# Optimization experiments

Hardware: AMD Instinct MI355X
Metric: run time of the kernel (lower is better)

Reference implementation:

```python
import jax, jax.numpy as jnp
import numpy as np

N = 100_000      # n_nodes
E = 1_000_000    # n_edges (avg degree 10)
DIN = 64
DOUT = 64


def setup_inputs() -> dict:
    key = jax.random.key(0)
    k1, k2, k3, k4 = jax.random.split(key, 4)
    x = jax.random.normal(k1, (N, DIN), dtype=jnp.float32)
    edge_index = jax.random.randint(k2, (2, E), 0, N, dtype=jnp.int32)
    # GCNConv linear weight (glorot-ish scale) and bias
    W = jax.random.normal(k3, (DIN, DOUT), dtype=jnp.float32) * (1.0 / np.sqrt(DIN))
    b = jax.random.normal(k4, (DOUT,), dtype=jnp.float32) * 0.01
    return {"x": x, "edge_index": edge_index, "W": W, "b": b}


def reference(x, edge_index, W, b):
    n = x.shape[0]
    # linear transform first (PyG GCNConv: x = self.lin(x))
    h = x @ W  # [N, DOUT]
    # add self-loops
    loop = jnp.arange(n, dtype=edge_index.dtype)
    row = jnp.concatenate([edge_index[0], loop])  # source j
    col = jnp.concatenate([edge_index[1], loop])  # target i
    # symmetric normalization: deg computed on target index (PyG gcn_norm)
    deg = jax.ops.segment_sum(jnp.ones(row.shape[0], dtype=h.dtype), col, num_segments=n)
    dinv = jnp.where(deg > 0, jax.lax.rsqrt(deg), 0.0)
    norm = dinv[row] * dinv[col]  # [E+N]
    # gather source features, scale, scatter-add to targets
    out = jax.ops.segment_sum(norm[:, None] * h[row], col, num_segments=n)
    out = out + b
    # dropout is identity in eval mode; act = relu
    return jax.nn.relu(out)
```

## Files before the change

kernel.cpp:

```cpp
#include <hip/hip_runtime.h>
#include <hip/hip_bf16.h>

#define F 64
#define BK 128
#define CAP 4096
#define ECAP 2048
#define PA_BLOCKS 256

typedef __attribute__((ext_vector_type(8))) short bf16x8;
typedef __attribute__((ext_vector_type(4))) float f32x4;

static __device__ inline short f2bf_bits(float f) {
    union { __hip_bfloat16 b; short s; } cv;
    cv.b = __float2bfloat16(f);
    return cv.s;
}

__global__ void __launch_bounds__(256)
k1_kernel(const float* __restrict__ x, const float* __restrict__ W,
          __hip_bfloat16* __restrict__ h,
          const int* __restrict__ row, const int* __restrict__ col,
          int* __restrict__ bcursor, unsigned* __restrict__ bin,
          int n, int e, int ngemm, int K, int chunk) {
    __shared__ int smem[2048];
    int tid = threadIdx.x;

    if ((int)blockIdx.x < ngemm) {
        short* Wb = (short*)smem;
        for (int i = tid; i < F * F; i += 256) Wb[i] = f2bf_bits(W[i]);
        __syncthreads();
        int lane = tid & 63;
        int wv = tid >> 6;
        int quad = lane >> 4;
        int l16 = lane & 15;

        bf16x8 bfr[2][4];
#pragma unroll
        for (int ks = 0; ks < 2; ++ks)
#pragma unroll
            for (int nb = 0; nb < 4; ++nb) {
                bf16x8 f;
#pragma unroll
                for (int j = 0; j < 8; ++j)
                    f[j] = Wb[(ks * 32 + quad * 8 + j) * F + nb * 16 + l16];
                bfr[ks][nb] = f;
            }

        int blockbase = blockIdx.x * 256;
#pragma unroll
        for (int mt = 0; mt < 4; ++mt) {
            int trow = blockbase + (wv * 4 + mt) * 16;
            int ar = trow + l16;
            bf16x8 af0, af1;
            if (ar < n) {
                const float* xr = x + (size_t)ar * F + quad * 8;
                float4 v0 = ((const float4*)xr)[0];
                float4 v1 = ((const float4*)xr)[1];
                float4 v2 = ((const float4*)(xr + 32))[0];
                float4 v3 = ((const float4*)(xr + 32))[1];
                af0[0] = f2bf_bits(v0.x); af0[1] = f2bf_bits(v0.y);
                af0[2] = f2bf_bits(v0.z); af0[3] = f2bf_bits(v0.w);
                af0[4] = f2bf_bits(v1.x); af0[5] = f2bf_bits(v1.y);
                af0[6] = f2bf_bits(v1.z); af0[7] = f2bf_bits(v1.w);
                af1[0] = f2bf_bits(v2.x); af1[1] = f2bf_bits(v2.y);
                af1[2] = f2bf_bits(v2.z); af1[3] = f2bf_bits(v2.w);
                af1[4] = f2bf_bits(v3.x); af1[5] = f2bf_bits(v3.y);
                af1[6] = f2bf_bits(v3.z); af1[7] = f2bf_bits(v3.w);
            } else {
                af0 = (bf16x8)0; af1 = (bf16x8)0;
            }
            f32x4 acc[4];
#pragma unroll
            for (int nb = 0; nb < 4; ++nb) {
                acc[nb] = (f32x4)0.f;
                acc[nb] = __builtin_amdgcn_mfma_f32_16x16x32_bf16(af0, bfr[0][nb], acc[nb], 0, 0, 0);
                acc[nb] = __builtin_amdgcn_mfma_f32_16x16x32_bf16(af1, bfr[1][nb], acc[nb], 0, 0, 0);
            }
#pragma unroll
            for (int nb = 0; nb < 4; ++nb)
#pragma unroll
                for (int r = 0; r < 4; ++r) {
                    int grow = trow + quad * 4 + r;
                    if (grow < n)
                        h[(size_t)grow * F + nb * 16 + l16] = __float2bfloat16(acc[nb][r]);
                }
        }
    } else {
        int* lh = smem;
        int* lbase = smem + 1024;
        int pb = blockIdx.x - ngemm;
        int s = pb * chunk;
        int lim = min(s + chunk, e);
        for (int i = tid; i < K; i += 256) lh[i] = 0;
        __syncthreads();
        for (int i = s + tid; i < lim; i += 256) atomicAdd(&lh[col[i] >> 7], 1);
        __syncthreads();
        for (int i = tid; i < K; i += 256) {
            int c = lh[i];
            lbase[i] = c ? atomicAdd(&bcursor[i], c) : 0;
            lh[i] = 0;
        }
        __syncthreads();
        for (int i = s + tid; i < lim; i += 256) {
            int d = col[i];
            int bkt = d >> 7;
            int off = lbase[bkt] + atomicAdd(&lh[bkt], 1);
            if (off < CAP)
                bin[(size_t)bkt * CAP + off] = ((unsigned)row[i] << 7) | ((unsigned)d & 127u);
        }
    }
}

__global__ void __launch_bounds__(256)
dinv_kernel(const unsigned* __restrict__ bin, const int* __restrict__ bcursor,
            float* __restrict__ dinv, int n) {
    __shared__ int lcnt[BK];
    int tid = threadIdx.x;
    int b = blockIdx.x;
    int s = b * CAP;
    int cnt = min(bcursor[b], ECAP);
    if (tid < BK) lcnt[tid] = 0;
    __syncthreads();
    for (int p = tid; p < cnt; p += 256) atomicAdd(&lcnt[bin[s + p] & 127u], 1);
    __syncthreads();
    if (tid < BK) {
        int node = (b << 7) + tid;
        if (node < n) dinv[node] = rsqrtf((float)(lcnt[tid] + 1));
    }
}

__global__ void __launch_bounds__(256)
gather_kernel(const unsigned* __restrict__ bin, const int* __restrict__ bcursor,
              const float* __restrict__ dinv, const __hip_bfloat16* __restrict__ h,
              const float* __restrict__ bias, float* __restrict__ out, int n) {
    __shared__ unsigned ebuf[ECAP];
    __shared__ int ssrc[ECAP];
    __shared__ int lcnt[BK];
    __shared__ int sstart[BK];
    __shared__ int lcur[BK];
    __shared__ int sc[BK];
    __shared__ float sdinv[BK];
    int tid = threadIdx.x;
    int b = blockIdx.x;
    int base = b << 7;
    int s = b * CAP;
    int cnt = min(bcursor[b], ECAP);

    if (tid < BK) lcnt[tid] = 0;
    __syncthreads();
    for (int p = tid; p < cnt; p += 256) {
        unsigned u = bin[s + p];
        ebuf[p] = u;
        atomicAdd(&lcnt[u & 127u], 1);
    }
    __syncthreads();
    if (tid < BK) sc[tid] = lcnt[tid];
    __syncthreads();
    for (int off = 1; off < BK; off <<= 1) {
        int t = (tid < BK && tid >= off) ? sc[tid - off] : 0;
        __syncthreads();
        if (tid < BK) sc[tid] += t;
        __syncthreads();
    }
    if (tid < BK) {
        int c = lcnt[tid];
        int st = sc[tid] - c;
        sstart[tid] = st;
        lcur[tid] = st;
        sdinv[tid] = rsqrtf((float)(c + 1));
    }
    __syncthreads();
    for (int p = tid; p < cnt; p += 256) {
        unsigned u = ebuf[p];
        int pos = atomicAdd(&lcur[u & 127u], 1);
        ssrc[pos] = (int)(u >> 7);
    }
    __syncthreads();

    int g = tid >> 3, cl = tid & 7;
    const uint4* h8 = (const uint4*)h;
#pragma unroll
    for (int r = 0; r < 4; ++r) {
        int ln = r * 32 + g;
        int node = base + ln;
        if (node >= n) continue;
        float di = sdinv[ln];
        float a0 = 0.f, a1 = 0.f, a2 = 0.f, a3 = 0.f,
              a4 = 0.f, a5 = 0.f, a6 = 0.f, a7 = 0.f;
        {
            uint4 hv = h8[(size_t)node * 8 + cl];
            a0 = di * __uint_as_float(hv.x << 16);
            a1 = di * __uint_as_float(hv.x & 0xffff0000u);
            a2 = di * __uint_as_float(hv.y << 16);
            a3 = di * __uint_as_float(hv.y & 0xffff0000u);
            a4 = di * __uint_as_float(hv.z << 16);
            a5 = di * __uint_as_float(hv.z & 0xffff0000u);
            a6 = di * __uint_as_float(hv.w << 16);
            a7 = di * __uint_as_float(hv.w & 0xffff0000u);
        }
        int p = sstart[ln];
        int pend = p + lcnt[ln];
        for (; p < pend; ++p) {
            int src = ssrc[p];
            float w = dinv[src];
            uint4 hv = h8[(size_t)src * 8 + cl];
            a0 += w * __uint_as_float(hv.x << 16);
            a1 += w * __uint_as_float(hv.x & 0xffff0000u);
            a2 += w * __uint_as_float(hv.y << 16);
            a3 += w * __uint_as_float(hv.y & 0xffff0000u);
            a4 += w * __uint_as_float(hv.z << 16);
            a5 += w * __uint_as_float(hv.z & 0xffff0000u);
            a6 += w * __uint_as_float(hv.w << 16);
            a7 += w * __uint_as_float(hv.w & 0xffff0000u);
        }
        float4 b0 = ((const float4*)bias)[cl * 2];
        float4 b1 = ((const float4*)bias)[cl * 2 + 1];
        float4 r0, r1;
        r0.x = di * a0 + b0.x; r0.y = di * a1 + b0.y;
        r0.z = di * a2 + b0.z; r0.w = di * a3 + b0.w;
        r1.x = di * a4 + b1.x; r1.y = di * a5 + b1.y;
        r1.z = di * a6 + b1.z; r1.w = di * a7 + b1.w;
        r0.x = r0.x > 0.f ? r0.x : 0.f; r0.y = r0.y > 0.f ? r0.y : 0.f;
        r0.z = r0.z > 0.f ? r0.z : 0.f; r0.w = r0.w > 0.f ? r0.w : 0.f;
        r1.x = r1.x > 0.f ? r1.x : 0.f; r1.y = r1.y > 0.f ? r1.y : 0.f;
        r1.z = r1.z > 0.f ? r1.z : 0.f; r1.w = r1.w > 0.f ? r1.w : 0.f;
        ((float4*)out)[(size_t)node * 16 + cl * 2] = r0;
        ((float4*)out)[(size_t)node * 16 + cl * 2 + 1] = r1;
    }
}

extern "C" void kernel_launch(void* const* d_in, const int* in_sizes, int n_in,
                              void* d_out, int out_size, void* d_ws, size_t ws_size,
                              hipStream_t stream) {
    const float* x = (const float*)d_in[0];
    const int* ei  = (const int*)d_in[1];
    const float* W = (const float*)d_in[2];
    const float* b = (const float*)d_in[3];
    float* out = (float*)d_out;

    int n = in_sizes[0] / F;
    int e = in_sizes[1] / 2;
    const int* row = ei;
    const int* col = ei + e;
    int K = (n + BK - 1) / BK;

    __hip_bfloat16* h = (__hip_bfloat16*)d_ws;
    unsigned* bin = (unsigned*)((char*)d_ws + (size_t)n * F * 2);
    float* dinv   = (float*)(bin + (size_t)K * CAP);
    int* bcursor  = (int*)(dinv + n);

    hipMemsetAsync(bcursor, 0, 1024 * sizeof(int), stream);

    int ngemm = (n + 255) / 256;
    int chunk = (e + PA_BLOCKS - 1) / PA_BLOCKS;
    k1_kernel<<<ngemm + PA_BLOCKS, 256, 0, stream>>>(x, W, h, row, col, bcursor,
                                                     bin, n, e, ngemm, K, chunk);

    dinv_kernel<<<K, 256, 0, stream>>>(bin, bcursor, dinv, n);

    gather_kernel<<<K, 256, 0, stream>>>(bin, bcursor, dinv, h, b, out, n);
}
```

Baseline: 145.2 us.

## Compute degrees with global atomics in partition pass and drop dinv kernel

Node in-degrees are now counted with global atomicAdd on a deg array during the edge partitioning pass, which removes the separate dinv kernel and its launch. The gather kernel computes each source's normalization weight once per edge while bucketing into shared memory, storing (src, weight) pairs, so the inner loop no longer does a dependent global load of dinv. This adds one million global atomics to the partition pass, a larger memset, and doubles the shared-memory footprint of the edge list.

After: 172.5 us. 18.8% more time.

```diff
diff --git a/kernel.cpp b/kernel.cpp
--- a/kernel.cpp
+++ b/kernel.cpp
@@ -20,7 +20,8 @@
 k1_kernel(const float* __restrict__ x, const float* __restrict__ W,
           __hip_bfloat16* __restrict__ h,
           const int* __restrict__ row, const int* __restrict__ col,
-          int* __restrict__ bcursor, unsigned* __restrict__ bin,
+          int* __restrict__ bcursor, int* __restrict__ deg,
+          unsigned* __restrict__ bin,
           int n, int e, int ngemm, int K, int chunk) {
     __shared__ int smem[2048];
     int tid = threadIdx.x;
@@ -93,7 +94,11 @@
         int lim = min(s + chunk, e);
         for (int i = tid; i < K; i += 256) lh[i] = 0;
         __syncthreads();
-        for (int i = s + tid; i < lim; i += 256) atomicAdd(&lh[col[i] >> 7], 1);
+        for (int i = s + tid; i < lim; i += 256) {
+            int d = col[i];
+            atomicAdd(&lh[d >> 7], 1);
+            atomicAdd(&deg[d], 1);
+        }
         __syncthreads();
         for (int i = tid; i < K; i += 256) {
             int c = lh[i];
@@ -112,29 +117,11 @@
 }
 
 __global__ void __launch_bounds__(256)
-dinv_kernel(const unsigned* __restrict__ bin, const int* __restrict__ bcursor,
-            float* __restrict__ dinv, int n) {
-    __shared__ int lcnt[BK];
-    int tid = threadIdx.x;
-    int b = blockIdx.x;
-    int s = b * CAP;
-    int cnt = min(bcursor[b], ECAP);
-    if (tid < BK) lcnt[tid] = 0;
-    __syncthreads();
-    for (int p = tid; p < cnt; p += 256) atomicAdd(&lcnt[bin[s + p] & 127u], 1);
-    __syncthreads();
-    if (tid < BK) {
-        int node = (b << 7) + tid;
-        if (node < n) dinv[node] = rsqrtf((float)(lcnt[tid] + 1));
-    }
-}
-
-__global__ void __launch_bounds__(256)
 gather_kernel(const unsigned* __restrict__ bin, const int* __restrict__ bcursor,
-              const float* __restrict__ dinv, const __hip_bfloat16* __restrict__ h,
+              const int* __restrict__ deg, const __hip_bfloat16* __restrict__ h,
               const float* __restrict__ bias, float* __restrict__ out, int n) {
     __shared__ unsigned ebuf[ECAP];
-    __shared__ int ssrc[ECAP];
+    __shared__ uint2 sent[ECAP];
     __shared__ int lcnt[BK];
     __shared__ int sstart[BK];
     __shared__ int lcur[BK];
@@ -167,13 +154,16 @@
         int st = sc[tid] - c;
         sstart[tid] = st;
         lcur[tid] = st;
-        sdinv[tid] = rsqrtf((float)(c + 1));
+        int node = base + tid;
+        sdinv[tid] = (node < n) ? rsqrtf((float)(deg[node] + 1)) : 0.f;
     }
     __syncthreads();
     for (int p = tid; p < cnt; p += 256) {
         unsigned u = ebuf[p];
+        int src = (int)(u >> 7);
+        float w = rsqrtf((float)(deg[src] + 1));
         int pos = atomicAdd(&lcur[u & 127u], 1);
-        ssrc[pos] = (int)(u >> 7);
+        sent[pos] = make_uint2((unsigned)src, __float_as_uint(w));
     }
     __syncthreads();
 
@@ -201,9 +191,9 @@
         int p = sstart[ln];
         int pend = p + lcnt[ln];
         for (; p < pend; ++p) {
-            int src = ssrc[p];
-            float w = dinv[src];
-            uint4 hv = h8[(size_t)src * 8 + cl];
+            uint2 ew = sent[p];
+            float w = __uint_as_float(ew.y);
+            uint4 hv = h8[(size_t)ew.x * 8 + cl];
             a0 += w * __uint_as_float(hv.x << 16);
             a1 += w * __uint_as_float(hv.x & 0xffff0000u);
             a2 += w * __uint_as_float(hv.y << 16);
@@ -246,17 +236,15 @@
 
     __hip_bfloat16* h = (__hip_bfloat16*)d_ws;
     unsigned* bin = (unsigned*)((char*)d_ws + (size_t)n * F * 2);
-    float* dinv   = (float*)(bin + (size_t)K * CAP);
-    int* bcursor  = (int*)(dinv + n);
-
-    hipMemsetAsync(bcursor, 0, 1024 * sizeof(int), stream);
+    int* bcursor  = (int*)(bin + (size_t)K * CAP);
+    int* deg      = bcursor + 1024;
+
+    hipMemsetAsync(bcursor, 0, (size_t)(1024 + n) * sizeof(int), stream);
 
     int ngemm = (n + 255) / 256;
     int chunk = (e + PA_BLOCKS - 1) / PA_BLOCKS;
     k1_kernel<<<ngemm + PA_BLOCKS, 256, 0, stream>>>(x, W, h, row, col, bcursor,
-                                                     bin, n, e, ngemm, K, chunk);
-
-    dinv_kernel<<<K, 256, 0, stream>>>(bin, bcursor, dinv, n);
-
-    gather_kernel<<<K, 256, 0, stream>>>(bin, bcursor, dinv, h, b, out, n);
-}
+                                                     deg, bin, n, e, ngemm, K, chunk);
+
+    gather_kernel<<<K, 256, 0, stream>>>(bin, bcursor, deg, h, b, out, n);
+}
```
